# Performance work log

Hardware: AMD Instinct MI355X
Metric: run time of the kernel (lower is better)

Reference implementation:

```python
import jax, jax.numpy as jnp
import numpy as np
from jax import lax

VOCAB = 12000
EMB = 512
RNN = 512
FEATS = 4096
SEQ_LEN = 15


def setup_inputs() -> dict:
    key = jax.random.key(0)
    ks = jax.random.split(key, 10)
    B = 1024
    s = 0.05
    return {
        "img_features": jax.random.normal(ks[0], (B, FEATS), jnp.float32),
        "W_feats": jax.random.normal(ks[1], (EMB, FEATS), jnp.float32) * s,
        "b_feats": jax.random.normal(ks[2], (EMB,), jnp.float32) * s,
        "W_ih": jax.random.normal(ks[3], (4 * RNN, EMB), jnp.float32) * s,
        "W_hh": jax.random.normal(ks[4], (4 * RNN, RNN), jnp.float32) * s,
        "b_ih": jax.random.normal(ks[5], (4 * RNN,), jnp.float32) * s,
        "b_hh": jax.random.normal(ks[6], (4 * RNN,), jnp.float32) * s,
        "emb": jax.random.normal(ks[7], (VOCAB, EMB), jnp.float32) * s,
        "W_out": jax.random.normal(ks[8], (VOCAB - 2, RNN), jnp.float32) * s,
        "b_out": jax.random.normal(ks[9], (VOCAB - 2,), jnp.float32) * s,
    }


def reference(img_features, W_feats, b_feats, W_ih, W_hh, b_ih, b_hh, emb, W_out, b_out):
    B = img_features.shape[0]

    def lstm_cell(x, h, c):
        # torch.nn.LSTMCell: gates ordered i, f, g, o
        gates = x @ W_ih.T + b_ih + h @ W_hh.T + b_hh
        i, f, g, o = jnp.split(gates, 4, axis=1)
        c_new = jax.nn.sigmoid(f) * c + jax.nn.sigmoid(i) * jnp.tanh(g)
        h_new = jax.nn.sigmoid(o) * jnp.tanh(c_new)
        return h_new, c_new

    # image feature embedding + ReLU, then prime the LSTM with it
    img_vec = jax.nn.relu(img_features @ W_feats.T + b_feats)  # [B, 512]
    h = jnp.zeros((B, RNN), img_features.dtype)
    c = jnp.zeros((B, RNN), img_features.dtype)
    h, c = lstm_cell(img_vec, h, c)

    def step(carry, _):
        h, c, words = carry
        x = emb[words]                     # [B, 512] embedding lookup
        h, c = lstm_cell(x, h, c)
        logits = h @ W_out.T + b_out       # [B, VOCAB-2]
        idx = jnp.argmax(logits, axis=1).astype(jnp.int32)
        return (h, c, idx + 2), idx

    words0 = jnp.ones((B,), jnp.int32)  # START token = 1
    _, seq = lax.scan(step, (h, c, words0), None, length=SEQ_LEN)
    return seq.T  # [B, SEQ_LEN] greedy-decoded token ids
```

## Files before the change

### kernel.cpp

```cpp
#include <hip/hip_runtime.h>
#include <stdint.h>

#define BATCH  1024
#define SEQLEN 15
#define NGATE  2048
#define NVOCAB 11998
#define FEATS  4096

typedef __attribute__((ext_vector_type(8)))  short  s8v;
typedef __attribute__((ext_vector_type(16))) float  f32x16;
typedef __attribute__((ext_vector_type(8)))  unsigned short us8;

__device__ __forceinline__ unsigned short f2bf(float f) {
    unsigned u = __float_as_uint(f);
    u += 0x7FFFu + ((u >> 16) & 1u);
    return (unsigned short)(u >> 16);
}
__device__ __forceinline__ float bf2f(unsigned short h) {
    return __uint_as_float(((unsigned)h) << 16);
}
struct bfpair { unsigned short hi, lo; };
__device__ __forceinline__ bfpair split2v(float v) {
    bfpair r;
    r.hi = f2bf(v);
    r.lo = f2bf(v - bf2f(r.hi));
    return r;
}
__device__ __forceinline__ void split8(const float* __restrict__ s, us8& vh, us8& vl) {
    #pragma unroll
    for (int e = 0; e < 8; ++e) {
        bfpair q = split2v(s[e]);
        vh[e] = q.hi; vl[e] = q.lo;
    }
}

__device__ __forceinline__ void async_cp16(const void* g, void* l) {
    __builtin_amdgcn_global_load_lds(
        (const __attribute__((address_space(1))) unsigned int*)g,
        (__attribute__((address_space(3))) unsigned int*)l, 16, 0, 0);
}

__global__ void prep_wcat_blk(const float* __restrict__ W_ih, const float* __restrict__ W_hh,
                              const float* __restrict__ b_ih, const float* __restrict__ b_hh,
                              unsigned short* __restrict__ hi, unsigned short* __restrict__ lo,
                              float* __restrict__ bsum) {
    int idx = blockIdx.x * 256 + threadIdx.x;
    int kc = idx >> 11, row = idx & 2047;
    int k = kc << 3;
    const float* src = (k < 512) ? (W_ih + (size_t)row * 512 + k)
                                 : (W_hh + (size_t)row * 512 + (k - 512));
    us8 vh, vl; split8(src, vh, vl);
    *(us8*)(hi + (size_t)idx * 8) = vh;
    *(us8*)(lo + (size_t)idx * 8) = vl;
    if (idx < NGATE) bsum[idx] = b_ih[idx] + b_hh[idx];
}

__global__ void prep_blk(const float* __restrict__ src,
                         unsigned short* __restrict__ hi, unsigned short* __restrict__ lo,
                         int R, int K) {
    int row = blockIdx.x * 256 + threadIdx.x;
    if (row >= R) return;
    int kc = blockIdx.y;
    us8 vh, vl; split8(src + (size_t)row * K + (kc << 3), vh, vl);
    size_t o = ((size_t)kc * R + row) * 8;
    *(us8*)(hi + o) = vh;
    *(us8*)(lo + o) = vl;
}

template<int MODE>
__device__ __forceinline__ void mfma_blk_body(
    const unsigned short* __restrict__ Ahi, const unsigned short* __restrict__ Alo, int aRows,
    const unsigned short* __restrict__ Bhi, const unsigned short* __restrict__ Blo, int bRows,
    const float* __restrict__ bias,
    float* __restrict__ C, int ldc,
    unsigned long long* __restrict__ packed,
    int N, int K, size_t akstride, size_t bkstride, size_t czstride)
{
    __shared__ short smem[4 * 4 * 128 * 8];
    short* sAhi = smem;
    short* sAlo = smem + 4 * 128 * 8;
    short* sBhi = smem + 2 * 4 * 128 * 8;
    short* sBlo = smem + 3 * 4 * 128 * 8;

    const int kz = blockIdx.z;
    Ahi += kz * akstride;  Alo += kz * akstride;
    Bhi += kz * bkstride;  Blo += kz * bkstride;
    if (MODE == 3) C += kz * czstride;

    const int tid  = threadIdx.x;
    const int lane = tid & 63, wave = tid >> 6;
    const int wr = (wave & 1) * 64, wc = (wave >> 1) * 64;
    const int col = lane & 31, kh = lane >> 5;
    const int bm = blockIdx.y * 128, bn = blockIdx.x * 128;

    f32x16 acc[2][2] = {};

    for (int k0 = 0; k0 < K; k0 += 32) {
        const int kc0 = k0 >> 3;
        __syncthreads();
        #pragma unroll
        for (int p = 0; p < 2; ++p) {
            int s    = p * 4 + wave;
            int kc_l = s >> 1, rh = s & 1;
            int rl   = rh * 64 + lane;
            int lo_  = (kc_l * 128 + rh * 64) * 8;
            size_t ga = ((size_t)(kc0 + kc_l) * aRows + (bm + rl)) * 8;
            async_cp16(Ahi + ga, sAhi + lo_);
            async_cp16(Alo + ga, sAlo + lo_);
            int brow = bn + rl; if (brow > N - 1) brow = N - 1;
            size_t gb = ((size_t)(kc0 + kc_l) * bRows + brow) * 8;
            async_cp16(Bhi + gb, sBhi + lo_);
            async_cp16(Blo + gb, sBlo + lo_);
        }
        __syncthreads();

        #pragma unroll
        for (int st = 0; st < 2; ++st) {
            int off = (2 * st + kh) * 128 * 8;
            s8v ah0 = *(const s8v*)(sAhi + off + (wr + col) * 8);
            s8v ah1 = *(const s8v*)(sAhi + off + (wr + 32 + col) * 8);
            s8v al0 = *(const s8v*)(sAlo + off + (wr + col) * 8);
            s8v al1 = *(const s8v*)(sAlo + off + (wr + 32 + col) * 8);
            s8v bh0 = *(const s8v*)(sBhi + off + (wc + col) * 8);
            s8v bh1 = *(const s8v*)(sBhi + off + (wc + 32 + col) * 8);
            s8v bl0 = *(const s8v*)(sBlo + off + (wc + col) * 8);
            s8v bl1 = *(const s8v*)(sBlo + off + (wc + 32 + col) * 8);

            acc[0][0] = __builtin_amdgcn_mfma_f32_32x32x16_bf16(ah0, bh0, acc[0][0], 0, 0, 0);
            acc[0][1] = __builtin_amdgcn_mfma_f32_32x32x16_bf16(ah0, bh1, acc[0][1], 0, 0, 0);
            acc[1][0] = __builtin_amdgcn_mfma_f32_32x32x16_bf16(ah1, bh0, acc[1][0], 0, 0, 0);
            acc[1][1] = __builtin_amdgcn_mfma_f32_32x32x16_bf16(ah1, bh1, acc[1][1], 0, 0, 0);
            acc[0][0] = __builtin_amdgcn_mfma_f32_32x32x16_bf16(ah0, bl0, acc[0][0], 0, 0, 0);
            acc[0][1] = __builtin_amdgcn_mfma_f32_32x32x16_bf16(ah0, bl1, acc[0][1], 0, 0, 0);
            acc[1][0] = __builtin_amdgcn_mfma_f32_32x32x16_bf16(ah1, bl0, acc[1][0], 0, 0, 0);
            acc[1][1] = __builtin_amdgcn_mfma_f32_32x32x16_bf16(ah1, bl1, acc[1][1], 0, 0, 0);
            acc[0][0] = __builtin_amdgcn_mfma_f32_32x32x16_bf16(al0, bh0, acc[0][0], 0, 0, 0);
            acc[0][1] = __builtin_amdgcn_mfma_f32_32x32x16_bf16(al0, bh1, acc[0][1], 0, 0, 0);
            acc[1][0] = __builtin_amdgcn_mfma_f32_32x32x16_bf16(al1, bh0, acc[1][0], 0, 0, 0);
            acc[1][1] = __builtin_amdgcn_mfma_f32_32x32x16_bf16(al1, bh1, acc[1][1], 0, 0, 0);
        }
    }

    if (MODE == 3) {
        #pragma unroll
        for (int i = 0; i < 2; ++i)
            #pragma unroll
            for (int rg = 0; rg < 4; ++rg)
                #pragma unroll
                for (int rr = 0; rr < 4; ++rr) {
                    int reg = rg * 4 + rr;
                    int m = bm + wr + i * 32 + rr + rg * 8 + kh * 4;
                    #pragma unroll
                    for (int j = 0; j < 2; ++j) {
                        int n = bn + wc + j * 32 + col;
                        if (n < N) C[(size_t)m * ldc + n] = acc[i][j][reg];
                    }
                }
    } else {
        #pragma unroll
        for (int i = 0; i < 2; ++i)
            #pragma unroll
            for (int rg = 0; rg < 4; ++rg)
                #pragma unroll
                for (int rr = 0; rr < 4; ++rr) {
                    int reg = rg * 4 + rr;
                    int m = bm + wr + i * 32 + rr + rg * 8 + kh * 4;
                    unsigned long long best = 0ull;
                    #pragma unroll
                    for (int j = 0; j < 2; ++j) {
                        int n = bn + wc + j * 32 + col;
                        if (n < N) {
                            float v = acc[i][j][reg] + bias[n];
                            unsigned int u   = __float_as_uint(v);
                            unsigned int key = (u & 0x80000000u) ? ~u : (u | 0x80000000u);
                            unsigned long long pk =
                                ((unsigned long long)key << 32) |
                                (unsigned long long)(0xFFFFFFFFu - (unsigned)n);
                            best = (pk > best) ? pk : best;
                        }
                    }
                    #pragma unroll
                    for (int sdist = 1; sdist < 32; sdist <<= 1) {
                        unsigned long long o = __shfl_xor(best, sdist, 64);
                        best = (o > best) ? o : best;
                    }
                    if (col == 0) atomicMax(&packed[m], best);
                }
    }
}

__global__ __launch_bounds__(256) void k_gemm_feats(
    const unsigned short* Ahi, const unsigned short* Alo, int aRows,
    const unsigned short* Bhi, const unsigned short* Blo, int bRows,
    float* C, int ldc, int N, int K, size_t aks, size_t bks, size_t czs) {
    mfma_blk_body<3>(Ahi, Alo, aRows, Bhi, Blo, bRows, nullptr, C, ldc, nullptr, N, K, aks, bks, czs);
}
__global__ __launch_bounds__(256) void k_gemm_gates(
    const unsigned short* Ahi, const unsigned short* Alo, int aRows,
    const unsigned short* Bhi, const unsigned short* Blo, int bRows,
    float* C, int ldc, int N, int K, size_t aks, size_t bks, size_t czs) {
    mfma_blk_body<3>(Ahi, Alo, aRows, Bhi, Blo, bRows, nullptr, C, ldc, nullptr, N, K, aks, bks, czs);
}
__global__ __launch_bounds__(256) void k_logits_argmax(
    const unsigned short* Ahi, const unsigned short* Alo, int aRows,
    const unsigned short* Bhi, const unsigned short* Blo, int bRows,
    const float* bias, unsigned long long* packed, int N, int K) {
    mfma_blk_body<2>(Ahi, Alo, aRows, Bhi, Blo, bRows, bias, nullptr, 0, packed, N, K, 0, 0, 0);
}

__global__ void feats_reduce8(const float* __restrict__ part, const float* __restrict__ bias,
                              unsigned short* __restrict__ hi, unsigned short* __restrict__ lo) {
    int idx = blockIdx.x * 256 + threadIdx.x;
    int b = idx >> 6, kc = idx & 63;
    int n = kc << 3;
    float v[8];
    #pragma unroll
    for (int e = 0; e < 8; ++e) v[e] = bias[n + e];
    #pragma unroll
    for (int z = 0; z < 8; ++z) {
        const float* s = part + (size_t)z * 1024 * 512 + (size_t)b * 512 + n;
        #pragma unroll
        for (int e = 0; e < 8; ++e) v[e] += s[e];
    }
    us8 vh, vl;
    #pragma unroll
    for (int e = 0; e < 8; ++e) {
        bfpair q = split2v(fmaxf(v[e], 0.f));
        vh[e] = q.hi; vl[e] = q.lo;
    }
    size_t o = ((size_t)kc * 1024 + b) * 8;
    *(us8*)(hi + o) = vh;
    *(us8*)(lo + o) = vl;
}

template<bool PRIME>
__global__ void lstm_pw_blk(const float* __restrict__ g0, const float* __restrict__ g1,
                            const float* __restrict__ bsum, float* __restrict__ cbuf,
                            unsigned short* __restrict__ xh_hi, unsigned short* __restrict__ xh_lo,
                            unsigned long long* __restrict__ packed) {
    int idx = blockIdx.x * 256 + threadIdx.x;
    int b = idx >> 6, j8 = idx & 63;
    int j = j8 << 3;
    const float* g = g0 + (size_t)b * NGATE;
    float v[4][8];
    #pragma unroll
    for (int gt = 0; gt < 4; ++gt) {
        const float* s = g + gt * 512 + j;
        const float* bs = bsum + gt * 512 + j;
        #pragma unroll
        for (int e = 0; e < 8; ++e) v[gt][e] = s[e] + bs[e];
    }
    if (g1) {
        const float* h2 = g1 + (size_t)b * NGATE;
        #pragma unroll
        for (int gt = 0; gt < 4; ++gt) {
            const float* s = h2 + gt * 512 + j;
            #pragma unroll
            for (int e = 0; e < 8; ++e) v[gt][e] += s[e];
        }
    }
    float* cb = cbuf + (size_t)b * 512 + j;
    us8 vh, vl;
    #pragma unroll
    for (int e = 0; e < 8; ++e) {
        float si = 1.f / (1.f + expf(-v[0][e]));
        float sf = 1.f / (1.f + expf(-v[1][e]));
        float tg = tanhf(v[2][e]);
        float so = 1.f / (1.f + expf(-v[3][e]));
        float cn = PRIME ? (si * tg) : (sf * cb[e] + si * tg);
        cb[e] = cn;
        bfpair q = split2v(so * tanhf(cn));
        vh[e] = q.hi; vl[e] = q.lo;
    }
    size_t o = ((size_t)(64 + j8) * 1024 + b) * 8;
    *(us8*)(xh_hi + o) = vh;
    *(us8*)(xh_lo + o) = vl;
    if (j8 == 0) packed[b] = 0ull;
}

template<int FIRST>
__global__ void gather_blk(const float* __restrict__ emb,
                           const unsigned long long* __restrict__ packed,
                           unsigned short* __restrict__ xh_hi, unsigned short* __restrict__ xh_lo,
                           int* __restrict__ out, int t) {
    int idx = blockIdx.x * 256 + threadIdx.x;
    int b = idx >> 6, kc = idx & 63;
    int word;
    if (FIRST) {
        word = 1;
    } else {
        unsigned long long p = packed[b];
        int id = (int)(0xFFFFFFFFu - (unsigned)(p & 0xFFFFFFFFull));
        word = id + 2;
        if (kc == 0) out[b * SEQLEN + (t - 1)] = id;
    }
    us8 vh, vl; split8(emb + (size_t)word * 512 + (kc << 3), vh, vl);
    size_t o = ((size_t)kc * 1024 + b) * 8;
    *(us8*)(xh_hi + o) = vh;
    *(us8*)(xh_lo + o) = vl;
}

__global__ void final_out(const unsigned long long* __restrict__ packed, int* __restrict__ out) {
    int b = blockIdx.x * 256 + threadIdx.x;
    if (b < BATCH) {
        unsigned long long p = packed[b];
        out[b * SEQLEN + (SEQLEN - 1)] = (int)(0xFFFFFFFFu - (unsigned)(p & 0xFFFFFFFFull));
    }
}

extern "C" void kernel_launch(void* const* d_in, const int* in_sizes, int n_in,
                              void* d_out, int out_size, void* d_ws, size_t ws_size,
                              hipStream_t stream) {
    const float* img     = (const float*)d_in[0];
    const float* W_feats = (const float*)d_in[1];
    const float* b_feats = (const float*)d_in[2];
    const float* W_ih    = (const float*)d_in[3];
    const float* W_hh    = (const float*)d_in[4];
    const float* b_ih    = (const float*)d_in[5];
    const float* b_hh    = (const float*)d_in[6];
    const float* emb     = (const float*)d_in[7];
    const float* W_out   = (const float*)d_in[8];
    const float* b_out   = (const float*)d_in[9];
    int* out = (int*)d_out;

    const size_t WCAT_H = (size_t)128 * 2048 * 8;
    const size_t WOUT_H = (size_t)64 * NVOCAB * 8;
    const size_t XH_H   = (size_t)128 * 1024 * 8;
    const size_t IMGV_H = (size_t)64 * 1024 * 8;

    char* p = (char*)d_ws;
    unsigned short* wcat_hi = (unsigned short*)p;  p += WCAT_H * 2;
    unsigned short* wcat_lo = (unsigned short*)p;  p += WCAT_H * 2;
    unsigned short* wout_hi = (unsigned short*)p;  p += WOUT_H * 2;
    unsigned short* wout_lo = (unsigned short*)p;  p += WOUT_H * 2;
    unsigned short* xh_hi   = (unsigned short*)p;  p += XH_H * 2;
    unsigned short* xh_lo   = (unsigned short*)p;  p += XH_H * 2;
    unsigned short* imgv_hi = (unsigned short*)p;  p += IMGV_H * 2;
    unsigned short* imgv_lo = (unsigned short*)p;  p += IMGV_H * 2;
    float* cbuf             = (float*)p;           p += (size_t)1024 * 512 * 4;
    float* bsum             = (float*)p;           p += (size_t)NGATE * 4;
    unsigned long long* packed = (unsigned long long*)p;  p += (size_t)1024 * 8;
    float* gates0           = (float*)p;           p += (size_t)1024 * NGATE * 4;
    float* gates1           = (float*)p;           p += (size_t)1024 * NGATE * 4;
    unsigned short* imgb_hi = wout_hi;
    unsigned short* imgb_lo = imgb_hi + (size_t)512 * 1024 * 8;
    unsigned short* wfb_hi  = imgb_lo + (size_t)512 * 1024 * 8;
    unsigned short* wfb_lo  = wfb_hi  + (size_t)512 * 512 * 8;
    float* partials = gates0;

    prep_wcat_blk<<<1024, 256, 0, stream>>>(W_ih, W_hh, b_ih, b_hh, wcat_hi, wcat_lo, bsum);
    prep_blk<<<dim3(4, 512), 256, 0, stream>>>(img,     imgb_hi, imgb_lo, 1024, FEATS);
    prep_blk<<<dim3(2, 512), 256, 0, stream>>>(W_feats, wfb_hi,  wfb_lo,  512,  FEATS);

    k_gemm_feats<<<dim3(4, 8, 8), 256, 0, stream>>>(
        imgb_hi, imgb_lo, 1024, wfb_hi, wfb_lo, 512,
        partials, 512, 512, 512,
        (size_t)64 * 1024 * 8, (size_t)64 * 512 * 8, (size_t)1024 * 512);
    feats_reduce8<<<256, 256, 0, stream>>>(partials, b_feats, imgv_hi, imgv_lo);

    prep_blk<<<dim3(47, 64), 256, 0, stream>>>(W_out, wout_hi, wout_lo, NVOCAB, 512);

    k_gemm_gates<<<dim3(16, 8, 1), 256, 0, stream>>>(
        imgv_hi, imgv_lo, 1024, wcat_hi, wcat_lo, 2048,
        gates0, NGATE, NGATE, 512, 0, 0, 0);
    lstm_pw_blk<true><<<256, 256, 0, stream>>>(gates0, nullptr, bsum, cbuf, xh_hi, xh_lo, packed);

    for (int t = 0; t < SEQLEN; ++t) {
        if (t == 0) gather_blk<1><<<256, 256, 0, stream>>>(emb, packed, xh_hi, xh_lo, out, t);
        else        gather_blk<0><<<256, 256, 0, stream>>>(emb, packed, xh_hi, xh_lo, out, t);

        k_gemm_gates<<<dim3(16, 8, 2), 256, 0, stream>>>(
            xh_hi, xh_lo, 1024, wcat_hi, wcat_lo, 2048,
            gates0, NGATE, NGATE, 512,
            (size_t)64 * 1024 * 8, (size_t)64 * 2048 * 8, (size_t)1024 * NGATE);
        lstm_pw_blk<false><<<256, 256, 0, stream>>>(gates0, gates1, bsum, cbuf, xh_hi, xh_lo, packed);

        k_logits_argmax<<<dim3(94, 8, 1), 256, 0, stream>>>(
            xh_hi + (size_t)64 * 1024 * 8, xh_lo + (size_t)64 * 1024 * 8, 1024,
            wout_hi, wout_lo, NVOCAB, b_out, packed, NVOCAB, 512);
    }
    final_out<<<4, 256, 0, stream>>>(packed, out);
}
```

Measured before the change: 1.845 ms.

## Fuse logits-argmax GEMM with next-step hidden-to-gates GEMM in one launch

```diff
diff --git a/kernel.cpp b/kernel.cpp
--- a/kernel.cpp
+++ b/kernel.cpp
@@ -69,29 +69,23 @@
 
 template<int MODE>
 __device__ __forceinline__ void mfma_blk_body(
+    short* smem,
     const unsigned short* __restrict__ Ahi, const unsigned short* __restrict__ Alo, int aRows,
     const unsigned short* __restrict__ Bhi, const unsigned short* __restrict__ Blo, int bRows,
     const float* __restrict__ bias,
     float* __restrict__ C, int ldc,
     unsigned long long* __restrict__ packed,
-    int N, int K, size_t akstride, size_t bkstride, size_t czstride)
+    int K, int bm, int bn)
 {
-    __shared__ short smem[4 * 4 * 128 * 8];
     short* sAhi = smem;
     short* sAlo = smem + 4 * 128 * 8;
     short* sBhi = smem + 2 * 4 * 128 * 8;
     short* sBlo = smem + 3 * 4 * 128 * 8;
 
-    const int kz = blockIdx.z;
-    Ahi += kz * akstride;  Alo += kz * akstride;
-    Bhi += kz * bkstride;  Blo += kz * bkstride;
-    if (MODE == 3) C += kz * czstride;
-
     const int tid  = threadIdx.x;
     const int lane = tid & 63, wave = tid >> 6;
     const int wr = (wave & 1) * 64, wc = (wave >> 1) * 64;
     const int col = lane & 31, kh = lane >> 5;
-    const int bm = blockIdx.y * 128, bn = blockIdx.x * 128;
 
     f32x16 acc[2][2] = {};
 
@@ -107,7 +101,7 @@
             size_t ga = ((size_t)(kc0 + kc_l) * aRows + (bm + rl)) * 8;
             async_cp16(Ahi + ga, sAhi + lo_);
             async_cp16(Alo + ga, sAlo + lo_);
-            int brow = bn + rl; if (brow > N - 1) brow = N - 1;
+            int brow = bn + rl; if (brow > bRows - 1) brow = bRows - 1;
             size_t gb = ((size_t)(kc0 + kc_l) * bRows + brow) * 8;
             async_cp16(Bhi + gb, sBhi + lo_);
             async_cp16(Blo + gb, sBlo + lo_);
@@ -125,7 +119,6 @@
             s8v bh1 = *(const s8v*)(sBhi + off + (wc + 32 + col) * 8);
             s8v bl0 = *(const s8v*)(sBlo + off + (wc + col) * 8);
             s8v bl1 = *(const s8v*)(sBlo + off + (wc + 32 + col) * 8);
-
             acc[0][0] = __builtin_amdgcn_mfma_f32_32x32x16_bf16(ah0, bh0, acc[0][0], 0, 0, 0);
             acc[0][1] = __builtin_amdgcn_mfma_f32_32x32x16_bf16(ah0, bh1, acc[0][1], 0, 0, 0);
             acc[1][0] = __builtin_amdgcn_mfma_f32_32x32x16_bf16(ah1, bh0, acc[1][0], 0, 0, 0);
@@ -153,7 +146,7 @@
                     #pragma unroll
                     for (int j = 0; j < 2; ++j) {
                         int n = bn + wc + j * 32 + col;
-                        if (n < N) C[(size_t)m * ldc + n] = acc[i][j][reg];
+                        if (n < bRows) C[(size_t)m * ldc + n] = acc[i][j][reg];
                     }
                 }
     } else {
@@ -169,7 +162,7 @@
                     #pragma unroll
                     for (int j = 0; j < 2; ++j) {
                         int n = bn + wc + j * 32 + col;
-                        if (n < N) {
+                        if (n < bRows) {
                             float v = acc[i][j][reg] + bias[n];
                             unsigned int u   = __float_as_uint(v);
                             unsigned int key = (u & 0x80000000u) ? ~u : (u | 0x80000000u);
@@ -189,23 +182,48 @@
     }
 }
 
-__global__ __launch_bounds__(256) void k_gemm_feats(
-    const unsigned short* Ahi, const unsigned short* Alo, int aRows,
-    const unsigned short* Bhi, const unsigned short* Blo, int bRows,
-    float* C, int ldc, int N, int K, size_t aks, size_t bks, size_t czs) {
-    mfma_blk_body<3>(Ahi, Alo, aRows, Bhi, Blo, bRows, nullptr, C, ldc, nullptr, N, K, aks, bks, czs);
-}
-__global__ __launch_bounds__(256) void k_gemm_gates(
-    const unsigned short* Ahi, const unsigned short* Alo, int aRows,
-    const unsigned short* Bhi, const unsigned short* Blo, int bRows,
-    float* C, int ldc, int N, int K, size_t aks, size_t bks, size_t czs) {
-    mfma_blk_body<3>(Ahi, Alo, aRows, Bhi, Blo, bRows, nullptr, C, ldc, nullptr, N, K, aks, bks, czs);
-}
-__global__ __launch_bounds__(256) void k_logits_argmax(
-    const unsigned short* Ahi, const unsigned short* Alo, int aRows,
-    const unsigned short* Bhi, const unsigned short* Blo, int bRows,
-    const float* bias, unsigned long long* packed, int N, int K) {
-    mfma_blk_body<2>(Ahi, Alo, aRows, Bhi, Blo, bRows, bias, nullptr, 0, packed, N, K, 0, 0, 0);
+__global__ __launch_bounds__(256) void k_combined(
+    const unsigned short* __restrict__ h_hi, const unsigned short* __restrict__ h_lo,
+    const unsigned short* __restrict__ wout_hi, const unsigned short* __restrict__ wout_lo,
+    const unsigned short* __restrict__ whh_hi, const unsigned short* __restrict__ whh_lo,
+    const float* __restrict__ b_out, float* __restrict__ gates0,
+    unsigned long long* __restrict__ packed) {
+    __shared__ short smem[16384];
+    int id = blockIdx.x;
+    if (id < 768) {
+        int xcd = id & 7, slot = id >> 3;
+        int bn_t = xcd * 12 + (slot % 12);
+        int bm_t = slot / 12;
+        mfma_blk_body<2>(smem, h_hi, h_lo, 1024, wout_hi, wout_lo, NVOCAB,
+                         b_out, nullptr, 0, packed, 512, bm_t * 128, bn_t * 128);
+    } else {
+        int g = id - 768;
+        mfma_blk_body<3>(smem, h_hi, h_lo, 1024, whh_hi, whh_lo, NGATE,
+                         nullptr, gates0, NGATE, nullptr, 512,
+                         (g >> 4) * 128, (g & 15) * 128);
+    }
+}
+
+__global__ __launch_bounds__(256) void k_gates(
+    const unsigned short* __restrict__ Ahi, const unsigned short* __restrict__ Alo,
+    const unsigned short* __restrict__ Bhi, const unsigned short* __restrict__ Blo,
+    float* __restrict__ C) {
+    __shared__ short smem[16384];
+    mfma_blk_body<3>(smem, Ahi, Alo, 1024, Bhi, Blo, NGATE, nullptr, C, NGATE,
+                     nullptr, 512, blockIdx.y * 128, blockIdx.x * 128);
+}
+
+__global__ __launch_bounds__(256) void k_feats(
+    const unsigned short* __restrict__ Ahi, const unsigned short* __restrict__ Alo,
+    const unsigned short* __restrict__ Bhi, const unsigned short* __restrict__ Blo,
+    float* __restrict__ C) {
+    __shared__ short smem[16384];
+    int kz = blockIdx.z;
+    mfma_blk_body<3>(smem,
+                     Ahi + (size_t)kz * 64 * 1024 * 8, Alo + (size_t)kz * 64 * 1024 * 8, 1024,
+                     Bhi + (size_t)kz * 64 * 512 * 8,  Blo + (size_t)kz * 64 * 512 * 8,  512,
+                     nullptr, C + (size_t)kz * 1024 * 512, 512, nullptr, 512,
+                     blockIdx.y * 128, blockIdx.x * 128);
 }
 
 __global__ void feats_reduce8(const float* __restrict__ part, const float* __restrict__ bias,
@@ -237,7 +255,8 @@
 __global__ void lstm_pw_blk(const float* __restrict__ g0, const float* __restrict__ g1,
                             const float* __restrict__ bsum, float* __restrict__ cbuf,
                             unsigned short* __restrict__ xh_hi, unsigned short* __restrict__ xh_lo,
-                            unsigned long long* __restrict__ packed) {
+                            unsigned long long* __restrict__ packed,
+                            int* __restrict__ out, int t) {
     int idx = blockIdx.x * 256 + threadIdx.x;
     int b = idx >> 6, j8 = idx & 63;
     int j = j8 << 3;
@@ -250,7 +269,7 @@
         #pragma unroll
         for (int e = 0; e < 8; ++e) v[gt][e] = s[e] + bs[e];
     }
-    if (g1) {
+    if (!PRIME) {
         const float* h2 = g1 + (size_t)b * NGATE;
         #pragma unroll
         for (int gt = 0; gt < 4; ++gt) {
@@ -275,24 +294,25 @@
     size_t o = ((size_t)(64 + j8) * 1024 + b) * 8;
     *(us8*)(xh_hi + o) = vh;
     *(us8*)(xh_lo + o) = vl;
-    if (j8 == 0) packed[b] = 0ull;
+    if (j8 == 0) {
+        if (!PRIME && t > 0) {
+            unsigned long long p = packed[b];
+            out[b * SEQLEN + (t - 1)] = (int)(0xFFFFFFFFu - (unsigned)(p & 0xFFFFFFFFull));
+        }
+        packed[b] = 0ull;
+    }
 }
 
 template<int FIRST>
 __global__ void gather_blk(const float* __restrict__ emb,
                            const unsigned long long* __restrict__ packed,
-                           unsigned short* __restrict__ xh_hi, unsigned short* __restrict__ xh_lo,
-                           int* __restrict__ out, int t) {
+                           unsigned short* __restrict__ xh_hi, unsigned short* __restrict__ xh_lo) {
     int idx = blockIdx.x * 256 + threadIdx.x;
     int b = idx >> 6, kc = idx & 63;
-    int word;
-    if (FIRST) {
-        word = 1;
-    } else {
+    int word = 1;
+    if (!FIRST) {
         unsigned long long p = packed[b];
-        int id = (int)(0xFFFFFFFFu - (unsigned)(p & 0xFFFFFFFFull));
-        word = id + 2;
-        if (kc == 0) out[b * SEQLEN + (t - 1)] = id;
+        word = (int)(0xFFFFFFFFu - (unsigned)(p & 0xFFFFFFFFull)) + 2;
     }
     us8 vh, vl; split8(emb + (size_t)word * 512 + (kc << 3), vh, vl);
     size_t o = ((size_t)kc * 1024 + b) * 8;
@@ -348,36 +368,33 @@
     unsigned short* wfb_lo  = wfb_hi  + (size_t)512 * 512 * 8;
     float* partials = gates0;
 
+    const unsigned short* whh_hi = wcat_hi + (size_t)64 * 2048 * 8;
+    const unsigned short* whh_lo = wcat_lo + (size_t)64 * 2048 * 8;
+    const unsigned short* h_hi   = xh_hi + (size_t)64 * 1024 * 8;
+    const unsigned short* h_lo   = xh_lo + (size_t)64 * 1024 * 8;
+
     prep_wcat_blk<<<1024, 256, 0, stream>>>(W_ih, W_hh, b_ih, b_hh, wcat_hi, wcat_lo, bsum);
     prep_blk<<<dim3(4, 512), 256, 0, stream>>>(img,     imgb_hi, imgb_lo, 1024, FEATS);
     prep_blk<<<dim3(2, 512), 256, 0, stream>>>(W_feats, wfb_hi,  wfb_lo,  512,  FEATS);
 
-    k_gemm_feats<<<dim3(4, 8, 8), 256, 0, stream>>>(
-        imgb_hi, imgb_lo, 1024, wfb_hi, wfb_lo, 512,
-        partials, 512, 512, 512,
-        (size_t)64 * 1024 * 8, (size_t)64 * 512 * 8, (size_t)1024 * 512);
+    k_feats<<<dim3(4, 8, 8), 256, 0, stream>>>(imgb_hi, imgb_lo, wfb_hi, wfb_lo, partials);
     feats_reduce8<<<256, 256, 0, stream>>>(partials, b_feats, imgv_hi, imgv_lo);
 
     prep_blk<<<dim3(47, 64), 256, 0, stream>>>(W_out, wout_hi, wout_lo, NVOCAB, 512);
 
-    k_gemm_gates<<<dim3(16, 8, 1), 256, 0, stream>>>(
-        imgv_hi, imgv_lo, 1024, wcat_hi, wcat_lo, 2048,
-        gates0, NGATE, NGATE, 512, 0, 0, 0);
-    lstm_pw_blk<true><<<256, 256, 0, stream>>>(gates0, nullptr, bsum, cbuf, xh_hi, xh_lo, packed);
+    k_gates<<<dim3(16, 8), 256, 0, stream>>>(imgv_hi, imgv_lo, wcat_hi, wcat_lo, gates0);
+    lstm_pw_blk<true><<<256, 256, 0, stream>>>(gates0, nullptr, bsum, cbuf,
+                                               xh_hi, xh_lo, packed, out, 0);
+    k_gates<<<dim3(16, 8), 256, 0, stream>>>(h_hi, h_lo, whh_hi, whh_lo, gates0);
 
     for (int t = 0; t < SEQLEN; ++t) {
-        if (t == 0) gather_blk<1><<<256, 256, 0, stream>>>(emb, packed, xh_hi, xh_lo, out, t);
-        else        gather_blk<0><<<256, 256, 0, stream>>>(emb, packed, xh_hi, xh_lo, out, t);
-
-        k_gemm_gates<<<dim3(16, 8, 2), 256, 0, stream>>>(
-            xh_hi, xh_lo, 1024, wcat_hi, wcat_lo, 2048,
-            gates0, NGATE, NGATE, 512,
-            (size_t)64 * 1024 * 8, (size_t)64 * 2048 * 8, (size_t)1024 * NGATE);
-        lstm_pw_blk<false><<<256, 256, 0, stream>>>(gates0, gates1, bsum, cbuf, xh_hi, xh_lo, packed);
-
-        k_logits_argmax<<<dim3(94, 8, 1), 256, 0, stream>>>(
-            xh_hi + (size_t)64 * 1024 * 8, xh_lo + (size_t)64 * 1024 * 8, 1024,
-            wout_hi, wout_lo, NVOCAB, b_out, packed, NVOCAB, 512);
+        if (t == 0) gather_blk<1><<<256, 256, 0, stream>>>(emb, packed, xh_hi, xh_lo);
+        else        gather_blk<0><<<256, 256, 0, stream>>>(emb, packed, xh_hi, xh_lo);
+        k_gates<<<dim3(16, 8), 256, 0, stream>>>(xh_hi, xh_lo, wcat_hi, wcat_lo, gates1);
+        lstm_pw_blk<false><<<256, 256, 0, stream>>>(gates0, gates1, bsum, cbuf,
+                                                    xh_hi, xh_lo, packed, out, t);
+        k_combined<<<896, 256, 0, stream>>>(h_hi, h_lo, wout_hi, wout_lo,
+                                            whh_hi, whh_lo, b_out, gates0, packed);
     }
     final_out<<<4, 256, 0, stream>>>(packed, out);
 }
```

New measurement: 2.169 ms. 17.6% more time.
